# Kernel tuning notes

Measured on AMD Instinct MI355X. Metric: run time of the kernel, lower is better.

## Reference

```python
import jax, jax.numpy as jnp
import numpy as np

U, I, E = 50000, 100000, 1600000
D, H, HID, B = 64, 8, 8, 16384
ALPHA = 0.2  # leaky relu slope


def setup_inputs() -> dict:
    key = jax.random.key(0)
    ks = jax.random.split(key, 12)
    return {
        "userIdx": jax.random.randint(ks[0], (B,), 0, U),
        "itemIdx": jax.random.randint(ks[1], (B,), 0, I),
        "edge_u": jax.random.randint(ks[2], (E,), 0, U),
        "edge_i": jax.random.randint(ks[3], (E,), 0, I),
        "uEmbd": jax.random.normal(ks[4], (U, D), dtype=jnp.float32) * 0.01,
        "iEmbd": jax.random.normal(ks[5], (I, D), dtype=jnp.float32) * 0.01,
        "Wu_h": jax.random.normal(ks[6], (H, D, HID), dtype=jnp.float32) * 0.18,
        "Wi_h": jax.random.normal(ks[7], (H, D, HID), dtype=jnp.float32) * 0.18,
        "a_h": jax.random.normal(ks[8], (H, 2 * HID), dtype=jnp.float32) * 0.3,
        "Wu_out": jax.random.normal(ks[9], (H * HID, D), dtype=jnp.float32) * 0.15,
        "Wi_out": jax.random.normal(ks[10], (H * HID, D), dtype=jnp.float32) * 0.15,
        "a_out": jax.random.normal(ks[11], (2 * D,), dtype=jnp.float32) * 0.1,
    }


def _leaky(x):
    return jnp.where(x >= 0, x, ALPHA * x)


def _gat_layer(fu, fi, Wu, Wi, a, edge_u, edge_i):
    # fu:[U,in], fi:[I,in], Wu/Wi:[in,out], a:[2*out]
    u_h = fu @ Wu  # [U,out]
    i_h = fi @ Wi  # [I,out]
    out = Wu.shape[1]
    # a . cat(u_h[eu], i_h[ei]) decomposed into per-node scores then edge gather
    su = u_h @ a[:out]  # [U]
    si = i_h @ a[out:]  # [I]
    e = jnp.exp(-_leaky(su[edge_u] + si[edge_i]))  # [E]
    rowsum = jax.ops.segment_sum(e, edge_u, num_segments=U)  # [U]
    colsum = jax.ops.segment_sum(e, edge_i, num_segments=I)  # [I]
    # users aggregate items they interacted with
    agg_i = jax.ops.segment_sum(e[:, None] * i_h[edge_i], edge_u, num_segments=U)  # [U,out]
    u_p = u_h + agg_i / jnp.where(rowsum == 0, 1.0, rowsum)[:, None]
    # items aggregate users (nan from empty cols -> 0, as in original)
    agg_u = jax.ops.segment_sum(e[:, None] * u_h[edge_u], edge_i, num_segments=I)  # [I,out]
    att_u = jnp.where((colsum > 0)[:, None], agg_u / jnp.where(colsum == 0, 1.0, colsum)[:, None], 0.0)
    i_p = i_h + att_u
    return u_p, i_p


def reference(userIdx, itemIdx, edge_u, edge_i, uEmbd, iEmbd, Wu_h, Wi_h, a_h, Wu_out, Wi_out, a_out):
    # eval mode: all dropout layers are identity
    fu, fi = uEmbd, iEmbd
    head = jax.vmap(lambda Wu, Wi, a: _gat_layer(fu, fi, Wu, Wi, a, edge_u, edge_i))
    u_ps, i_ps = head(Wu_h, Wi_h, a_h)  # [H,U,HID], [H,I,HID]
    # concat=True heads: elu then concatenate along feature dim (head-major columns)
    hu = jax.nn.elu(u_ps).transpose(1, 0, 2).reshape(U, H * HID)
    hi = jax.nn.elu(i_ps).transpose(1, 0, 2).reshape(I, H * HID)
    u_p, i_p = _gat_layer(hu, hi, Wu_out, Wi_out, a_out, edge_u, edge_i)
    u_f = jax.nn.elu(u_p)  # final F.elu in SpUIGAT
    i_f = jax.nn.elu(i_p)
    return jnp.sum(u_f[userIdx] * i_f[itemIdx], axis=1)  # [B]
```

## Files before the change

kernel.cpp:

```cpp
#include <hip/hip_runtime.h>
#include <hip/hip_fp16.h>

#define U_N 50000
#define I_N 100000
#define E_N 1600000
#define B_N 16384
#define UI_N (U_N + I_N)
#define NB_U 782
#define NB_I 1563
#define NBK 586
#define CAP 16384
#define NBLD 256
#define CHUNK (E_N / NBLD)
#define COL_CAP 3300000
#define MAXACT 32768
#define FP8_SCALE 128.0f

typedef float f32x2 __attribute__((ext_vector_type(2)));

__global__ __launch_bounds__(1024) void k_build1(
    const int* __restrict__ eu, const int* __restrict__ ei,
    int* __restrict__ bcnt, int* __restrict__ ecnt, int* __restrict__ storage) {
  __shared__ int hist[NBK];
  __shared__ int pb16[NBK];
  __shared__ int gbase[NBK];
  __shared__ int loff[NBK];
  __shared__ short map16[1344];
  __shared__ int sc[1024];
  __shared__ int sorted[21504];
  int t = threadIdx.x;
  for (int b = t; b < NBK; b += 1024) { hist[b] = 0; loff[b] = 0; }
  __syncthreads();
  int e0 = blockIdx.x * CHUNK;
  int myu[7], myi[7];
#pragma unroll
  for (int k = 0; k < 7; k++) {
    myu[k] = -1;
    if (t + 1024 * k < CHUNK) {
      int e = e0 + t + 1024 * k;
      int u = eu[e], it = ei[e];
      myu[k] = u;
      myi[k] = it;
      atomicAdd(&hist[u >> 8], 1);
      atomicAdd(&hist[(U_N + it) >> 8], 1);
    }
  }
  __syncthreads();
  int ph = (t < NBK) ? ((hist[t] + 15) & ~15) : 0;
  sc[t] = ph;
  __syncthreads();
  int val = ph;
  for (int o = 1; o < 1024; o <<= 1) {
    int x = (t >= o) ? sc[t - o] : 0;
    __syncthreads();
    val += x;
    sc[t] = val;
    __syncthreads();
  }
  int total16 = sc[1023];
  if (t < NBK) {
    int myb = val - ph;
    pb16[t] = myb;
    gbase[t] = ph ? atomicAdd(&bcnt[t], ph) : 0;
    if (hist[t]) atomicAdd(&ecnt[t], hist[t]);
    for (int k = myb >> 4; k < (myb + ph) >> 4; k++) map16[k] = (short)t;
  }
  for (int j = t; j < total16; j += 1024) sorted[j] = -1;
  __syncthreads();
#pragma unroll
  for (int k = 0; k < 7; k++) {
    if (myu[k] >= 0) {
      int u = myu[k], it = myi[k];
      int k2 = U_N + it;
      int b1 = u >> 8;
      int p1 = pb16[b1] + atomicAdd(&loff[b1], 1);
      sorted[p1] = ((u & 255) << 18) | k2;
      int b2 = k2 >> 8;
      int p2 = pb16[b2] + atomicAdd(&loff[b2], 1);
      sorted[p2] = ((k2 & 255) << 18) | u;
    }
  }
  __syncthreads();
  for (int j = t; j < total16; j += 1024) {
    int b = map16[j >> 4];
    storage[(size_t)b * CAP + gbase[b] + (j - pb16[b])] = sorted[j];
  }
}

__device__ void build2_body(int b, const int* __restrict__ bcnt,
                            const int* __restrict__ ecnt,
                            const int* __restrict__ storage,
                            int* __restrict__ ptr, int* __restrict__ col,
                            int* smem) {
  int* c = smem;
  int* sc = smem + 256;
  int* pbl = smem + 512;
  int* cur = smem + 768;
  int* tot = smem + 1024;
  int* lcol = smem + 1040;
  int t = threadIdx.x;
  int pre = 0;
  for (int i = t; i < b; i += 256) pre += ecnt[i];
  sc[t] = pre;
  c[t] = 0;
  __syncthreads();
  for (int o = 128; o > 0; o >>= 1) {
    if (t < o) sc[t] += sc[t + o];
    __syncthreads();
  }
  int base = sc[0];
  __syncthreads();
  int n = bcnt[b];
  const int* s = storage + (size_t)b * CAP;
  for (int i = t; i < n; i += 256) {
    int e = s[i];
    if (e >= 0) atomicAdd(&c[e >> 18], 1);
  }
  __syncthreads();
  int deg = c[t];
  sc[t] = deg;
  __syncthreads();
  int val = deg;
  for (int o = 1; o < 256; o <<= 1) {
    int x = (t >= o) ? sc[t - o] : 0;
    __syncthreads();
    val += x;
    sc[t] = val;
    __syncthreads();
  }
  int myoff = val - deg;
  pbl[t] = myoff;
  cur[t] = 0;
  if (t == 255) tot[0] = val;
  int node = b * 256 + t;
  if (node < UI_N) ptr[node] = base + myoff;
  if (b == NBK - 1 && t == 255) ptr[UI_N] = base + val;
  __syncthreads();
  for (int i = t; i < n; i += 256) {
    int e = s[i];
    if (e >= 0) {
      int local = e >> 18;
      int pos = pbl[local] + atomicAdd(&cur[local], 1);
      lcol[pos] = e & 0x3FFFF;
    }
  }
  __syncthreads();
  int vt = tot[0];
  for (int i = t; i < vt; i += 256) col[base + i] = lcol[i];
}

__device__ __forceinline__ void flagc_body(int bid, const int* __restrict__ uIdx,
                                           const int* __restrict__ iIdx,
                                           int* __restrict__ flag, int* __restrict__ list,
                                           int* __restrict__ nm) {
  int b = bid * 256 + threadIdx.x;
  if (b < B_N) {
    int u = uIdx[b];
    if (atomicExch(&flag[u], 1) == 0) list[atomicAdd(nm, 1)] = u;
    int it = U_N + iIdx[b];
    if (atomicExch(&flag[it], 1) == 0) list[atomicAdd(nm, 1)] = it;
  }
}

__device__ __forceinline__ void mm2_body(
    int bid, const float* __restrict__ Xu32, const float* __restrict__ Xi32,
    const __half* __restrict__ X16,
    const float* __restrict__ Wu, const float* __restrict__ Wi,
    const float* __restrict__ a, int layer,
    __half* __restrict__ f16, unsigned char* __restrict__ f8,
    __half* __restrict__ s16, const int* __restrict__ flagp,
    float* Wl, float* Xs) {
  const bool isU = bid < NB_U;
  const int N = isU ? U_N : I_N;
  const int base = (isU ? bid : bid - NB_U) * 64;
  const int gofs = isU ? 0 : U_N;
  const float* W = isU ? Wu : Wi;
  const int aoff = (layer == 1) ? (isU ? 0 : 8) : (isU ? 0 : 64);
  int t = threadIdx.x;

  if (layer == 1) {
#pragma unroll
    for (int k = 0; k < 4; k++) {
      int i = t + 256 * k;
      int h = i >> 7, d = (i >> 1) & 63, half = i & 1;
      float4 v = *(const float4*)(W + h * 512 + d * 8 + half * 4);
      *(float4*)(Wl + d * 64 + h * 8 + half * 4) = v;
    }
    const float* X = isU ? Xu32 : Xi32;
#pragma unroll
    for (int k = 0; k < 4; k++) {
      int i = t + 256 * k;
      int r = i >> 4, ch = i & 15;
      int node = base + r;
      float4 v = make_float4(0.f, 0.f, 0.f, 0.f);
      if (node < N) v = *(const float4*)(X + (size_t)node * 64 + ch * 4);
      *(float4*)(Xs + r * 64 + ch * 4) = v;
    }
  } else {
#pragma unroll
    for (int k = 0; k < 4; k++) {
      int i = t + 256 * k;
      *(float4*)(Wl + i * 4) = *(const float4*)(W + i * 4);
    }
#pragma unroll
    for (int k = 0; k < 4; k++) {
      int i = t + 256 * k;
      int r = i >> 4, ch = i & 15;
      int node = base + r;
      float4 v = make_float4(0.f, 0.f, 0.f, 0.f);
      if (node < N) {
        const __half2* hp = (const __half2*)(X16 + (size_t)(gofs + node) * 64 + ch * 4);
        float2 f0 = __half22float2(hp[0]);
        float2 f1 = __half22float2(hp[1]);
        v = make_float4(f0.x, f0.y, f1.x, f1.y);
      }
      *(float4*)(Xs + r * 64 + ch * 4) = v;
    }
  }
  __syncthreads();

  const int c0 = t & 31;
  const int rb = t >> 5;
  float acc0[8], acc1[8];
#pragma unroll
  for (int k = 0; k < 8; k++) { acc0[k] = 0.f; acc1[k] = 0.f; }

  for (int d0 = 0; d0 < 64; d0 += 4) {
    float2 wA = *(float2*)(Wl + (d0 + 0) * 64 + 2 * c0);
    float2 wB = *(float2*)(Wl + (d0 + 1) * 64 + 2 * c0);
    float2 wC = *(float2*)(Wl + (d0 + 2) * 64 + 2 * c0);
    float2 wD = *(float2*)(Wl + (d0 + 3) * 64 + 2 * c0);
#pragma unroll
    for (int k = 0; k < 8; k++) {
      float4 x = *(float4*)(Xs + (rb + 8 * k) * 64 + d0);
      acc0[k] += x.x * wA.x + x.y * wB.x + x.z * wC.x + x.w * wD.x;
      acc1[k] += x.x * wA.y + x.y * wB.y + x.z * wC.y + x.w * wD.y;
    }
  }

  float av0, av1;
  if (layer == 1) {
    int h = c0 >> 2, j = 2 * (c0 & 3);
    av0 = a[h * 16 + aoff + j];
    av1 = a[h * 16 + aoff + j + 1];
  } else {
    av0 = a[aoff + 2 * c0];
    av1 = a[aoff + 2 * c0 + 1];
  }
#pragma unroll
  for (int k = 0; k < 8; k++) {
    int node = base + rb + 8 * k;
    float s = acc0[k] * av0 + acc1[k] * av1;
    s += __shfl_xor(s, 1);
    s += __shfl_xor(s, 2);
    if (layer != 1) {
      s += __shfl_xor(s, 4);
      s += __shfl_xor(s, 8);
      s += __shfl_xor(s, 16);
    }
    if (node < N) {
      int gn = gofs + node;
      if (layer == 1 || flagp[gn]) {
        float2 f;
        f.x = acc0[k];
        f.y = acc1[k];
        *(__half2*)(f16 + (size_t)gn * 64 + 2 * c0) = __float22half2_rn(f);
      }
      int pk = __builtin_amdgcn_cvt_pk_fp8_f32(acc0[k] * FP8_SCALE,
                                               acc1[k] * FP8_SCALE, 0, false);
      *(unsigned short*)(f8 + (size_t)gn * 64 + 2 * c0) = (unsigned short)pk;
      if (layer == 1) {
        if ((c0 & 3) == 0) s16[gn * 8 + (c0 >> 2)] = __float2half_rn(s);
      } else {
        if (c0 == 0) s16[gn] = __float2half_rn(s);
      }
    }
  }
}

__global__ __launch_bounds__(256) void k_fused2(
    const int* __restrict__ bcnt, const int* __restrict__ ecnt,
    const int* __restrict__ storage,
    int* __restrict__ ptr, int* __restrict__ col,
    const int* __restrict__ uIdx, const int* __restrict__ iIdx,
    int* __restrict__ flag, int* __restrict__ list, int* __restrict__ nm,
    const float* __restrict__ uEmbd, const float* __restrict__ iEmbd,
    const float* __restrict__ Wu, const float* __restrict__ Wi,
    const float* __restrict__ a, __half* __restrict__ fA,
    unsigned char* __restrict__ fA8, __half* __restrict__ s16) {
  __shared__ __align__(16) int smem_i[11296];
  int bx = blockIdx.x;
  if (bx < NBK) {
    build2_body(bx, bcnt, ecnt, storage, ptr, col, smem_i);
  } else if (bx < NBK + 64) {
    flagc_body(bx - NBK, uIdx, iIdx, flag, list, nm);
  } else {
    float* s = (float*)smem_i;
    mm2_body(bx - NBK - 64, uEmbd, iEmbd, nullptr, Wu, Wi, a, 1, fA, fA8, s16,
             nullptr, s, s + 4096);
  }
}

__global__ __launch_bounds__(256) void k_mm2(
    const __half* __restrict__ X16, const float* __restrict__ Wu,
    const float* __restrict__ Wi, const float* __restrict__ a,
    __half* __restrict__ f16, unsigned char* __restrict__ f8,
    __half* __restrict__ s2, const int* __restrict__ flag) {
  __shared__ __align__(16) float smv[8192];
  mm2_body(blockIdx.x, nullptr, nullptr, X16, Wu, Wi, a, 2, f16, f8, s2, flag,
           smv, smv + 4096);
}

template <int LAYER>
__device__ __forceinline__ void agg_body(
    const int* __restrict__ ptr, const int* __restrict__ col,
    const unsigned char* __restrict__ f8,
    const __half* __restrict__ fA,
    __half* __restrict__ fB,
    const __half* __restrict__ sc,
    const int* __restrict__ list, const int* __restrict__ nm) {
  int gid = blockIdx.x * blockDim.x + threadIdx.x;
  int wv = gid >> 6;
  int l = threadIdx.x & 63;
  int half = l >> 5;
  int idx = wv * 2 + half;
  bool act = true;
  int n;
  if (LAYER == 2) {
    act = idx < *nm;
    n = act ? list[idx] : 0;
  } else {
    n = idx;
  }
  int lh = l & 31;
  int g = lh >> 3;
  int cc = lh & 7;

  int beg = ptr[n], endA = ptr[n + 1];
  int deg = act ? (endA - beg) : 0;
  unsigned coff = ((unsigned)(beg + g)) << 2;
  const unsigned begb = (unsigned)beg << 2;
  const unsigned f8sh = (unsigned)cc << 3;
  const unsigned ssh = (LAYER == 1) ? ((unsigned)cc << 1) : 0u;
  float sself = (LAYER == 1) ? __half2float(sc[(size_t)n * 8 + cc])
                             : __half2float(sc[n]);
  f32x2 acc2[4];
#pragma unroll
  for (int k = 0; k < 4; k++) acc2[k] = (f32x2){0.f, 0.f};
  float wsum = 0.f;
  const char* colc = (const char*)col;
  const char* f8c = (const char*)f8;
  const char* scc = (const char*)sc;

  auto edge = [&](unsigned off) {
    int nb = *(const int*)(colc + off);
    unsigned so = (LAYER == 1) ? (((unsigned)nb << 4) + ssh) : ((unsigned)nb << 1);
    float x = sself + __half2float(*(const __half*)(scc + so));
    int2 r = *(const int2*)(f8c + (((unsigned)nb << 6) + f8sh));
    float w = __expf(-fmaxf(x, 0.2f * x));
    wsum += w;
    f32x2 w2 = {w, w};
    acc2[0] += w2 * __builtin_amdgcn_cvt_pk_f32_fp8((unsigned)r.x, false);
    acc2[1] += w2 * __builtin_amdgcn_cvt_pk_f32_fp8((unsigned)r.x, true);
    acc2[2] += w2 * __builtin_amdgcn_cvt_pk_f32_fp8((unsigned)r.y, false);
    acc2[3] += w2 * __builtin_amdgcn_cvt_pk_f32_fp8((unsigned)r.y, true);
  };
  auto edgem = [&](unsigned off, bool valid) {
    unsigned o = valid ? off : begb;
    int nb = *(const int*)(colc + o);
    unsigned so = (LAYER == 1) ? (((unsigned)nb << 4) + ssh) : ((unsigned)nb << 1);
    float x = sself + __half2float(*(const __half*)(scc + so));
    int2 r = *(const int2*)(f8c + (((unsigned)nb << 6) + f8sh));
    float w = valid ? __expf(-fmaxf(x, 0.2f * x)) : 0.f;
    wsum += w;
    f32x2 w2 = {w, w};
    acc2[0] += w2 * __builtin_amdgcn_cvt_pk_f32_fp8((unsigned)r.x, false);
    acc2[1] += w2 * __builtin_amdgcn_cvt_pk_f32_fp8((unsigned)r.x, true);
    acc2[2] += w2 * __builtin_amdgcn_cvt_pk_f32_fp8((unsigned)r.y, false);
    acc2[3] += w2 * __builtin_amdgcn_cvt_pk_f32_fp8((unsigned)r.y, true);
  };

  int q = deg >> 4;
  for (; q > 0; q--) {
    edge(coff);
    edge(coff + 16);
    edge(coff + 32);
    edge(coff + 48);
    coff += 64;
  }
  int rem = deg & 15;
  if (rem) {
    edgem(coff, g < rem);
    edgem(coff + 16, (4 + g) < rem);
    if (rem > 8) {
      edgem(coff + 32, (8 + g) < rem);
      edgem(coff + 48, (12 + g) < rem);
    }
  }

#pragma unroll
  for (int k = 0; k < 4; k++) {
    f32x2 t;
    t.x = __shfl_xor(acc2[k].x, 8);
    t.y = __shfl_xor(acc2[k].y, 8);
    acc2[k] += t;
    t.x = __shfl_xor(acc2[k].x, 16);
    t.y = __shfl_xor(acc2[k].y, 16);
    acc2[k] += t;
  }
  wsum += __shfl_xor(wsum, 8);
  wsum += __shfl_xor(wsum, 16);

  if (act) {
    float inv = (deg > 0) ? 1.f / (wsum * FP8_SCALE) : 0.f;
    f32x2 a2;
    if (g == 0) a2 = acc2[0];
    else if (g == 1) a2 = acc2[1];
    else if (g == 2) a2 = acc2[2];
    else a2 = acc2[3];
    size_t boff = (size_t)n * 64 + cc * 8 + 2 * g;
    float2 sf = __half22float2(*(const __half2*)(fA + boff));
    float v0 = sf.x + a2.x * inv;
    float v1 = sf.y + a2.y * inv;
    v0 = (v0 > 0.f) ? v0 : (__expf(v0) - 1.f);
    v1 = (v1 > 0.f) ? v1 : (__expf(v1) - 1.f);
    *(__half2*)(fB + boff) = __floats2half2_rn(v0, v1);
  }
}

__global__ __launch_bounds__(256) void k_aggL1(
    const int* __restrict__ ptr, const int* __restrict__ col,
    const unsigned char* __restrict__ f8, const __half* __restrict__ fA,
    __half* __restrict__ fB, const __half* __restrict__ s16) {
  agg_body<1>(ptr, col, f8, fA, fB, s16, nullptr, nullptr);
}

__global__ __launch_bounds__(256) void k_aggL2(
    const int* __restrict__ ptr, const int* __restrict__ col,
    const unsigned char* __restrict__ f8, const __half* __restrict__ fA,
    __half* __restrict__ fB, const __half* __restrict__ s2,
    const int* __restrict__ list, const int* __restrict__ nm) {
  agg_body<2>(ptr, col, f8, fA, fB, s2, list, nm);
}

__global__ void k_dot(const int* __restrict__ uIdx, const int* __restrict__ iIdx,
                      const __half* __restrict__ u_f, const __half* __restrict__ i_f,
                      float* __restrict__ out) {
  int t = threadIdx.x;
  int pair = blockIdx.x * 32 + (t >> 3);
  int cc = t & 7;
  float4 ra = *(const float4*)(u_f + (size_t)uIdx[pair] * 64 + cc * 8);
  float4 rb = *(const float4*)(i_f + (size_t)iIdx[pair] * 64 + cc * 8);
  const __half* ha = (const __half*)&ra;
  const __half* hb = (const __half*)&rb;
  float v = 0.f;
#pragma unroll
  for (int k = 0; k < 8; k++) v += (float)ha[k] * (float)hb[k];
  v += __shfl_xor(v, 1);
  v += __shfl_xor(v, 2);
  v += __shfl_xor(v, 4);
  if (cc == 0) out[pair] = v;
}

extern "C" void kernel_launch(void* const* d_in, const int* in_sizes, int n_in,
                              void* d_out, int out_size, void* d_ws, size_t ws_size,
                              hipStream_t stream) {
  const int* userIdx = (const int*)d_in[0];
  const int* itemIdx = (const int*)d_in[1];
  const int* edge_u = (const int*)d_in[2];
  const int* edge_i = (const int*)d_in[3];
  const float* uEmbd = (const float*)d_in[4];
  const float* iEmbd = (const float*)d_in[5];
  const float* Wu_h = (const float*)d_in[6];
  const float* Wi_h = (const float*)d_in[7];
  const float* a_h = (const float*)d_in[8];
  const float* Wu_out = (const float*)d_in[9];
  const float* Wi_out = (const float*)d_in[10];
  const float* a_out = (const float*)d_in[11];
  float* out = (float*)d_out;

  char* w = (char*)d_ws;
  size_t off = 0;
  auto alloc = [&](size_t bytes) -> void* {
    void* p = w + off;
    off += (bytes + 511) & ~(size_t)511;
    return p;
  };
  int* bcnt = (int*)alloc((size_t)(2 * NBK + 16 + UI_N) * 4);
  int* ecnt = bcnt + NBK;
  int* nm = bcnt + 2 * NBK;
  int* flag = bcnt + 2 * NBK + 16;
  int* ptr = (int*)alloc((size_t)(UI_N + 1) * 4);
  int* list = (int*)alloc((size_t)MAXACT * 4);
  int* col = (int*)alloc((size_t)COL_CAP * 4);
  __half* fA = (__half*)alloc((size_t)UI_N * 64 * 2);
  unsigned char* fA8 = (unsigned char*)alloc((size_t)UI_N * 64);
  __half* s16 = (__half*)alloc((size_t)UI_N * 8 * 2);
  __half* s2 = (__half*)alloc((size_t)UI_N * 2);
  size_t union_off = off;
  int* storage = (int*)alloc((size_t)NBK * CAP * 4);
  size_t end_storage = off;
  off = union_off;
  __half* fB = (__half*)alloc((size_t)UI_N * 64 * 2);
  if (off < end_storage) off = end_storage;

  hipMemsetAsync(bcnt, 0, (size_t)(2 * NBK + 16 + UI_N) * 4, stream);
  k_build1<<<NBLD, 1024, 0, stream>>>(edge_u, edge_i, bcnt, ecnt, storage);

  k_fused2<<<NBK + 64 + NB_U + NB_I, 256, 0, stream>>>(
      bcnt, ecnt, storage, ptr, col, userIdx, itemIdx, flag, list, nm,
      uEmbd, iEmbd, Wu_h, Wi_h, a_h, fA, fA8, s16);

  k_aggL1<<<UI_N * 32 / 256, 256, 0, stream>>>(ptr, col, fA8, fA, fB, s16);

  k_mm2<<<NB_U + NB_I, 256, 0, stream>>>(fB, Wu_out, Wi_out, a_out, fA, fA8, s2, flag);
  k_aggL2<<<MAXACT * 32 / 256, 256, 0, stream>>>(ptr, col, fA8, fA, fB, s2, list, nm);

  k_dot<<<B_N / 32, 256, 0, stream>>>(userIdx, itemIdx, fB, fB + (size_t)U_N * 64, out);
}
```

Baseline: 270.4 us.

## Halve edge-sort chunks, scatter CSR cols directly, prescale scores for exp2

The edge bucketing kernel now runs with twice as many blocks, each handling half the edges, so it needs less shared memory and gets more parallelism. The CSR build no longer stages columns in shared memory and writes them directly to global memory at their final slots, which drops a copy pass and lets k_fused2 use a smaller shared allocation that may raise occupancy. Attention scores are pre-multiplied by log2(e) so the aggregation kernels can call exp2f instead of __expf. The aggregation grid sizes are rewritten as UI_N/8 and MAXACT/8, which are the same values as before. Direct scattered col writes are less coalesced than the old staged copy.

New measurement: 280.2 us. 3.6% more time.

```diff
diff --git a/kernel.cpp b/kernel.cpp
--- a/kernel.cpp
+++ b/kernel.cpp
@@ -10,11 +10,12 @@
 #define NB_I 1563
 #define NBK 586
 #define CAP 16384
-#define NBLD 256
+#define NBLD 512
 #define CHUNK (E_N / NBLD)
 #define COL_CAP 3300000
 #define MAXACT 32768
 #define FP8_SCALE 128.0f
+#define LOG2E 1.44269504088896f
 
 typedef float f32x2 __attribute__((ext_vector_type(2)));
 
@@ -25,16 +26,16 @@
   __shared__ int pb16[NBK];
   __shared__ int gbase[NBK];
   __shared__ int loff[NBK];
-  __shared__ short map16[1344];
+  __shared__ short map16[960];
   __shared__ int sc[1024];
-  __shared__ int sorted[21504];
+  __shared__ int sorted[15104];
   int t = threadIdx.x;
   for (int b = t; b < NBK; b += 1024) { hist[b] = 0; loff[b] = 0; }
   __syncthreads();
   int e0 = blockIdx.x * CHUNK;
-  int myu[7], myi[7];
-#pragma unroll
-  for (int k = 0; k < 7; k++) {
+  int myu[4], myi[4];
+#pragma unroll
+  for (int k = 0; k < 4; k++) {
     myu[k] = -1;
     if (t + 1024 * k < CHUNK) {
       int e = e0 + t + 1024 * k;
@@ -68,7 +69,7 @@
   for (int j = t; j < total16; j += 1024) sorted[j] = -1;
   __syncthreads();
 #pragma unroll
-  for (int k = 0; k < 7; k++) {
+  for (int k = 0; k < 4; k++) {
     if (myu[k] >= 0) {
       int u = myu[k], it = myi[k];
       int k2 = U_N + it;
@@ -94,10 +95,8 @@
                             int* smem) {
   int* c = smem;
   int* sc = smem + 256;
-  int* pbl = smem + 512;
+  int* pb = smem + 512;
   int* cur = smem + 768;
-  int* tot = smem + 1024;
-  int* lcol = smem + 1040;
   int t = threadIdx.x;
   int pre = 0;
   for (int i = t; i < b; i += 256) pre += ecnt[i];
@@ -128,25 +127,21 @@
     sc[t] = val;
     __syncthreads();
   }
-  int myoff = val - deg;
-  pbl[t] = myoff;
+  int myPtr = base + (val - deg);
+  pb[t] = myPtr;
   cur[t] = 0;
-  if (t == 255) tot[0] = val;
   int node = b * 256 + t;
-  if (node < UI_N) ptr[node] = base + myoff;
+  if (node < UI_N) ptr[node] = myPtr;
   if (b == NBK - 1 && t == 255) ptr[UI_N] = base + val;
   __syncthreads();
   for (int i = t; i < n; i += 256) {
     int e = s[i];
     if (e >= 0) {
       int local = e >> 18;
-      int pos = pbl[local] + atomicAdd(&cur[local], 1);
-      lcol[pos] = e & 0x3FFFF;
-    }
-  }
-  __syncthreads();
-  int vt = tot[0];
-  for (int i = t; i < vt; i += 256) col[base + i] = lcol[i];
+      int slot = pb[local] + atomicAdd(&cur[local], 1);
+      col[slot] = e & 0x3FFFF;
+    }
+  }
 }
 
 __device__ __forceinline__ void flagc_body(int bid, const int* __restrict__ uIdx,
@@ -270,9 +265,9 @@
                                                acc1[k] * FP8_SCALE, 0, false);
       *(unsigned short*)(f8 + (size_t)gn * 64 + 2 * c0) = (unsigned short)pk;
       if (layer == 1) {
-        if ((c0 & 3) == 0) s16[gn * 8 + (c0 >> 2)] = __float2half_rn(s);
+        if ((c0 & 3) == 0) s16[gn * 8 + (c0 >> 2)] = __float2half_rn(s * LOG2E);
       } else {
-        if (c0 == 0) s16[gn] = __float2half_rn(s);
+        if (c0 == 0) s16[gn] = __float2half_rn(s * LOG2E);
       }
     }
   }
@@ -288,16 +283,15 @@
     const float* __restrict__ Wu, const float* __restrict__ Wi,
     const float* __restrict__ a, __half* __restrict__ fA,
     unsigned char* __restrict__ fA8, __half* __restrict__ s16) {
-  __shared__ __align__(16) int smem_i[11296];
+  __shared__ __align__(16) float smv[8192];
   int bx = blockIdx.x;
   if (bx < NBK) {
-    build2_body(bx, bcnt, ecnt, storage, ptr, col, smem_i);
+    build2_body(bx, bcnt, ecnt, storage, ptr, col, (int*)smv);
   } else if (bx < NBK + 64) {
     flagc_body(bx - NBK, uIdx, iIdx, flag, list, nm);
   } else {
-    float* s = (float*)smem_i;
     mm2_body(bx - NBK - 64, uEmbd, iEmbd, nullptr, Wu, Wi, a, 1, fA, fA8, s16,
-             nullptr, s, s + 4096);
+             nullptr, smv, smv + 4096);
   }
 }
 
@@ -357,7 +351,7 @@
     unsigned so = (LAYER == 1) ? (((unsigned)nb << 4) + ssh) : ((unsigned)nb << 1);
     float x = sself + __half2float(*(const __half*)(scc + so));
     int2 r = *(const int2*)(f8c + (((unsigned)nb << 6) + f8sh));
-    float w = __expf(-fmaxf(x, 0.2f * x));
+    float w = exp2f(-fmaxf(x, 0.2f * x));
     wsum += w;
     f32x2 w2 = {w, w};
     acc2[0] += w2 * __builtin_amdgcn_cvt_pk_f32_fp8((unsigned)r.x, false);
@@ -371,7 +365,7 @@
     unsigned so = (LAYER == 1) ? (((unsigned)nb << 4) + ssh) : ((unsigned)nb << 1);
     float x = sself + __half2float(*(const __half*)(scc + so));
     int2 r = *(const int2*)(f8c + (((unsigned)nb << 6) + f8sh));
-    float w = valid ? __expf(-fmaxf(x, 0.2f * x)) : 0.f;
+    float w = valid ? exp2f(-fmaxf(x, 0.2f * x)) : 0.f;
     wsum += w;
     f32x2 w2 = {w, w};
     acc2[0] += w2 * __builtin_amdgcn_cvt_pk_f32_fp8((unsigned)r.x, false);
@@ -511,10 +505,10 @@
       bcnt, ecnt, storage, ptr, col, userIdx, itemIdx, flag, list, nm,
       uEmbd, iEmbd, Wu_h, Wi_h, a_h, fA, fA8, s16);
 
-  k_aggL1<<<UI_N * 32 / 256, 256, 0, stream>>>(ptr, col, fA8, fA, fB, s16);
+  k_aggL1<<<UI_N / 8, 256, 0, stream>>>(ptr, col, fA8, fA, fB, s16);
 
   k_mm2<<<NB_U + NB_I, 256, 0, stream>>>(fB, Wu_out, Wi_out, a_out, fA, fA8, s2, flag);
-  k_aggL2<<<MAXACT * 32 / 256, 256, 0, stream>>>(ptr, col, fA8, fA, fB, s2, list, nm);
+  k_aggL2<<<MAXACT / 8, 256, 0, stream>>>(ptr, col, fA8, fA, fB, s2, list, nm);
 
   k_dot<<<B_N / 32, 256, 0, stream>>>(userIdx, itemIdx, fB, fB + (size_t)U_N * 64, out);
 }
```
